# Kernel tuning notes

Measured on AMD Instinct MI355X. Metric: run time of the kernel, lower is better.

## Reference

```python
import jax, jax.numpy as jnp
import numpy as np

B, K, G, C = 64, 4000, 200, 91
LAMBDA_BOX, LAMBDA_CLS, LAMBDA_OBJ = 5.0, 1.0, 1.0
EPS = 1e-9


def _make_boxes(key, lead_shape):
    k1, k2 = jax.random.split(key)
    tl = jax.random.uniform(k1, lead_shape + (2,)) * 0.7
    wh = jax.random.uniform(k2, lead_shape + (2,)) * 0.29 + 0.01
    return jnp.concatenate([tl, tl + wh], axis=-1)


def setup_inputs() -> dict:
    key = jax.random.key(0)
    ks = jax.random.split(key, 6)
    pred_boxes = _make_boxes(ks[0], (B, K))
    pred_obj_logits = jax.random.normal(ks[1], (B, K), dtype=jnp.float32)
    pred_cls_logits = jax.random.normal(ks[2], (B, K, C), dtype=jnp.float32)
    gt_boxes = _make_boxes(ks[3], (B, G))
    gt_labels = jax.random.randint(ks[4], (B, G), 0, C)
    n_gt = jax.random.randint(ks[5], (B,), 1, G + 1)
    gt_mask = jnp.arange(G)[None, :] < n_gt[:, None]
    return dict(pred_boxes=pred_boxes, pred_obj_logits=pred_obj_logits,
                pred_cls_logits=pred_cls_logits, gt_boxes=gt_boxes,
                gt_labels=gt_labels, gt_mask=gt_mask)


def _area(x):
    return jnp.clip(x[..., 2] - x[..., 0], 0.0) * jnp.clip(x[..., 3] - x[..., 1], 0.0)


def _pairwise_iou(a, b):
    # a: (K,4), b: (G,4) -> (K,G)
    tl = jnp.maximum(a[:, None, :2], b[None, :, :2])
    br = jnp.minimum(a[:, None, 2:], b[None, :, 2:])
    wh = jnp.clip(br - tl, 0.0)
    inter = wh[..., 0] * wh[..., 1]
    union = jnp.clip(_area(a)[:, None] + _area(b)[None, :] - inter, EPS)
    return inter / union


def _ciou_loss(pb, gb):
    # pb, gb: (M,4) matched pairs; elementwise CIoU loss = 1 - CIoU
    tl = jnp.maximum(pb[:, :2], gb[:, :2])
    br = jnp.minimum(pb[:, 2:], gb[:, 2:])
    wh = jnp.clip(br - tl, 0.0)
    inter = wh[:, 0] * wh[:, 1]
    iou = inter / jnp.clip(_area(pb) + _area(gb) - inter, EPS)
    px = (pb[:, 0] + pb[:, 2]) * 0.5
    py = (pb[:, 1] + pb[:, 3]) * 0.5
    tx = (gb[:, 0] + gb[:, 2]) * 0.5
    ty = (gb[:, 1] + gb[:, 3]) * 0.5
    rho2 = (px - tx) ** 2 + (py - ty) ** 2
    etl = jnp.minimum(pb[:, :2], gb[:, :2])
    ebr = jnp.maximum(pb[:, 2:], gb[:, 2:])
    c2 = jnp.clip((ebr[:, 0] - etl[:, 0]) ** 2 + (ebr[:, 1] - etl[:, 1]) ** 2, EPS)
    pw = jnp.clip(pb[:, 2] - pb[:, 0], EPS)
    ph = jnp.clip(pb[:, 3] - pb[:, 1], EPS)
    tw = jnp.clip(gb[:, 2] - gb[:, 0], EPS)
    th = jnp.clip(gb[:, 3] - gb[:, 1], EPS)
    v = (4.0 / jnp.pi ** 2) * (jnp.arctan(tw / th) - jnp.arctan(pw / ph)) ** 2
    alpha = jax.lax.stop_gradient(v / (1.0 - iou + v + EPS))  # torch.no_grad
    return 1.0 - (iou - rho2 / c2 - alpha * v)


def _greedy_match(iou0):
    # iou0: (K,G), invalid gt columns pre-masked to -1. Fixed min(K,G)-step
    # argmax-and-mask scan reproducing the torch greedy loop (break -> valid=False).
    Gd = iou0.shape[1]
    steps = min(iou0.shape[0], Gd)

    def step(m, _):
        flat = jnp.argmax(m)
        p = flat // Gd
        g = flat % Gd
        valid = m.reshape(-1)[flat] >= 0.0
        m2 = m.at[p, :].set(-1.0).at[:, g].set(-1.0)
        return jnp.where(valid, m2, m), (p, g, valid)

    _, (ps, gs, vs) = jax.lax.scan(step, iou0, None, length=steps)
    return ps, gs, vs


def _per_batch(pred_b, cls_b, gt_b, labels_b, mask_b):
    iou = jax.lax.stop_gradient(_pairwise_iou(pred_b, gt_b))  # matching is non-diff (.item() in torch)
    iou = jnp.where(mask_b[None, :], iou, -1.0)
    ps, gs, vs = _greedy_match(iou)
    vf = vs.astype(pred_b.dtype)
    n = jnp.sum(vf)
    denom = jnp.maximum(n, 1.0)
    pb = pred_b[ps]
    gb = gt_b[gs]
    lbox = jnp.sum(_ciou_loss(pb, gb) * vf) / denom
    logp = jax.nn.log_softmax(cls_b[ps], axis=-1)
    lce = -jnp.take_along_axis(logp, labels_b[gs][:, None], axis=1)[:, 0]
    lcls = jnp.sum(lce * vf) / denom
    obj_tgt = jnp.zeros((pred_b.shape[0],), pred_b.dtype).at[
        jnp.where(vs, ps, pred_b.shape[0])].set(1.0, mode='drop')
    return lbox, lcls, obj_tgt, n > 0.0


def reference(pred_boxes, pred_obj_logits, pred_cls_logits, gt_boxes, gt_labels, gt_mask):
    lbox_b, lcls_b, obj_tgt, has = jax.vmap(_per_batch)(
        pred_boxes, pred_cls_logits, gt_boxes, gt_labels, gt_mask)
    hf = has.astype(pred_boxes.dtype)
    nb = jnp.maximum(jnp.sum(hf), 1.0)
    loss_box = jnp.sum(lbox_b * hf) / nb
    loss_cls = jnp.sum(lcls_b * hf) / nb
    # BCEWithLogits(mean): softplus(x) - t*x
    loss_obj = jnp.mean(jax.nn.softplus(pred_obj_logits) - obj_tgt * pred_obj_logits)
    total = LAMBDA_BOX * loss_box + LAMBDA_CLS * loss_cls + LAMBDA_OBJ * loss_obj
    return total, loss_box, loss_cls, loss_obj
```

## Files before the change

kernel.cpp:

```cpp
#include <hip/hip_runtime.h>
#include <math.h>

#define B_ 64
#define K_ 4000
#define G_ 200
#define C_ 91
#define EPS_ 1e-9f
#define NW_ 16
#define DEPTH_ 24
typedef unsigned long long ull;

#define WS_FLAG 0
#define WS_PART 256
#define WS_CNT 1536
#define WS_MATCH 2048
#define WS_ROWUSED 53248
#define WS_TOP 327680

__device__ __forceinline__ float box_area(float4 a) {
#pragma clang fp contract(off)
  return fmaxf(a.z - a.x, 0.f) * fmaxf(a.w - a.y, 0.f);
}

__device__ __forceinline__ float iou_ab(float4 a, float aA, float4 b, float aB) {
#pragma clang fp contract(off)
  float tlx = fmaxf(a.x, b.x), tly = fmaxf(a.y, b.y);
  float brx = fminf(a.z, b.z), bry = fminf(a.w, b.w);
  float w = fmaxf(brx - tlx, 0.f), h = fmaxf(bry - tly, 0.f);
  float inter = w * h;
  float uni = fmaxf(aA + aB - inter, EPS_);
  return inter / uni;
}

__device__ __forceinline__ float ciou_loss(float4 p, float4 g) {
  float tlx = fmaxf(p.x, g.x), tly = fmaxf(p.y, g.y);
  float brx = fminf(p.z, g.z), bry = fminf(p.w, g.w);
  float w = fmaxf(brx - tlx, 0.f), h = fmaxf(bry - tly, 0.f);
  float inter = w * h;
  float areaP = fmaxf(p.z - p.x, 0.f) * fmaxf(p.w - p.y, 0.f);
  float areaG = fmaxf(g.z - g.x, 0.f) * fmaxf(g.w - g.y, 0.f);
  float iou = inter / fmaxf(areaP + areaG - inter, EPS_);
  float px = (p.x + p.z) * 0.5f, py = (p.y + p.w) * 0.5f;
  float tx = (g.x + g.z) * 0.5f, ty = (g.y + g.w) * 0.5f;
  float rho2 = (px - tx) * (px - tx) + (py - ty) * (py - ty);
  float ex = fmaxf(p.z, g.z) - fminf(p.x, g.x);
  float ey = fmaxf(p.w, g.w) - fminf(p.y, g.y);
  float c2 = fmaxf(ex * ex + ey * ey, EPS_);
  float pw = fmaxf(p.z - p.x, EPS_), ph = fmaxf(p.w - p.y, EPS_);
  float tw = fmaxf(g.z - g.x, EPS_), th = fmaxf(g.w - g.y, EPS_);
  float dat = atanf(tw / th) - atanf(pw / ph);
  float v = (4.0f / (float)(M_PI * M_PI)) * dat * dat;
  float alpha = v / ((1.f - iou) + v + EPS_);
  return 1.f - (iou - rho2 / c2 - alpha * v);
}

__global__ void kdetect(const unsigned char* m8, int* flag) {
  int b = threadIdx.x;
  int ok = 1;
  const unsigned char* r = m8 + b * G_;
  if (r[0] != 1) ok = 0;
  int seen0 = 0;
  for (int g = 0; g < G_; ++g) {
    unsigned char c = r[g];
    if (c > 1) { ok = 0; break; }
    if (c == 0) seen0 = 1;
    else if (seen0) { ok = 0; break; }
  }
  int all = __all(ok);
  if (b == 0) *flag = all ? 1 : 0;
}

__device__ __forceinline__ float block_sum(float v, float* s_red) {
  for (int off = 32; off > 0; off >>= 1) v += __shfl_xor(v, off);
  int lane = threadIdx.x & 63, wid = threadIdx.x >> 6;
  if (lane == 0) s_red[wid] = v;
  __syncthreads();
  float r = 0.f;
  if (wid == 0) {
    float t = (lane < NW_) ? s_red[lane] : 0.f;
    for (int off = 32; off > 0; off >>= 1) t += __shfl_xor(t, off);
    r = t;
  }
  __syncthreads();
  return r;
}

__device__ __forceinline__ ull wave_maxkey(ull k) {
  for (int off = 32; off > 0; off >>= 1) {
    ull o = __shfl_xor(k, off);
    if (o > k) k = o;
  }
  return k;
}

#define TOP8_INS(key)                                   \
  if ((key) > t7) {                                     \
    t7 = (key);                                         \
    ull tmp_;                                           \
    if (t7 > t6) { tmp_ = t6; t6 = t7; t7 = tmp_; }     \
    if (t6 > t5) { tmp_ = t5; t5 = t6; t6 = tmp_; }     \
    if (t5 > t4) { tmp_ = t4; t4 = t5; t5 = tmp_; }     \
    if (t4 > t3) { tmp_ = t3; t3 = t4; t4 = tmp_; }     \
    if (t3 > t2) { tmp_ = t2; t2 = t3; t3 = tmp_; }     \
    if (t2 > t1) { tmp_ = t1; t1 = t2; t2 = tmp_; }     \
    if (t1 > t0) { tmp_ = t0; t0 = t1; t1 = tmp_; }     \
  }

__global__ __launch_bounds__(1024) void kinit(const float* __restrict__ pred_boxes,
                                              const float* __restrict__ gt_boxes,
                                              const void* __restrict__ gt_mask,
                                              char* __restrict__ ws) {
  __shared__ float4 s_p[K_];
  const int blk = blockIdx.x;
  const int b = blk >> 3, oct = blk & 7;
  const int tid = threadIdx.x, lane = tid & 63, wid = tid >> 6;
  const int msk8 = *(const int*)(ws + WS_FLAG);
  const float4* p4 = (const float4*)pred_boxes + (size_t)b * K_;
  const float4* g4 = (const float4*)gt_boxes + (size_t)b * G_;

  for (int i = tid; i < K_; i += 1024) s_p[i] = p4[i];
  __syncthreads();

  ull* wtop = (ull*)(ws + WS_TOP);
  for (int cc = wid; cc < 25; cc += 16) {
    const int col = oct * 25 + cc;
    ull* dst = wtop + ((size_t)b * G_ + col) * DEPTH_;
    int v;
    if (msk8) v = ((const unsigned char*)gt_mask)[(size_t)b * G_ + col] != 0;
    else      v = ((const int*)gt_mask)[(size_t)b * G_ + col] != 0;
    if (!v) {
      for (int o = lane; o < DEPTH_; o += 64) dst[o] = 0ull;
      continue;
    }
    float4 gb = g4[col];
    float gA = box_area(gb);
    ull t0 = 0, t1 = 0, t2 = 0, t3 = 0, t4 = 0, t5 = 0, t6 = 0, t7 = 0;
    for (int k = lane; k < K_; k += 64) {
      float4 pb = s_p[k];
      float iou = iou_ab(pb, box_area(pb), gb, gA);
      ull e = ((ull)__float_as_uint(iou) << 12) | (ull)(4095 - k);
      TOP8_INS(e);
    }
    int supplied = 0, written = 0;
    for (int o = 0; o < DEPTH_; ++o) {
      ull m = wave_maxkey(t0);
      if (m == 0ull) break;
      int dn = 0;
      if (t0 == m) {
        t0 = t1; t1 = t2; t2 = t3; t3 = t4; t4 = t5; t5 = t6; t6 = t7; t7 = 0;
        if (++supplied == 8) dn = 1;
      }
      if (lane == 0) dst[o] = m;
      ++written;
      if (__any(dn)) break;
    }
    for (int o = written + lane; o < DEPTH_; o += 64) dst[o] = 0ull;
  }
}

__global__ __launch_bounds__(64) void kmatch(const float* __restrict__ pred_boxes,
                                             const float* __restrict__ gt_boxes,
                                             char* __restrict__ ws) {
  __shared__ float s_gx[G_], s_gy[G_], s_gz[G_], s_gw[G_], s_garea[G_];
  __shared__ unsigned char s_rowused[4096];
  __shared__ ull s_toplist[G_][DEPTH_ + 1];
  __shared__ int s_mp[G_];
  __shared__ unsigned short s_mg[G_];
  const int b = blockIdx.x;
  const int lane = threadIdx.x;
  const float4* p4 = (const float4*)pred_boxes + (size_t)b * K_;
  const float4* g4 = (const float4*)gt_boxes + (size_t)b * G_;

  for (int g = lane; g < G_; g += 64) {
    float4 gb = g4[g];
    s_gx[g] = gb.x; s_gy[g] = gb.y; s_gz[g] = gb.z; s_gw[g] = gb.w;
    s_garea[g] = box_area(gb);
  }
  for (int k = lane; k < 4096; k += 64) s_rowused[k] = 0;

  const ull* wtop = (const ull*)(ws + WS_TOP);
  ull key0 = 0, key1 = 0, key2 = 0, key3 = 0;
  int ptr0 = DEPTH_, ptr1 = DEPTH_, ptr2 = DEPTH_, ptr3 = DEPTH_;
  int cloc = 0;
#define SLOTLOAD(S)                                                         \
  { int col = S * 64 + lane;                                                \
    if (col < G_) {                                                         \
      const ull* src_ = wtop + ((size_t)b * G_ + col) * DEPTH_;             \
      ull h_ = src_[0];                                                     \
      s_toplist[col][0] = h_;                                               \
      _Pragma("unroll") for (int o = 1; o < DEPTH_; ++o)                    \
        s_toplist[col][o] = src_[o];                                        \
      if (h_ != 0ull) {                                                     \
        key##S = (h_ << 8) | (ull)(255 - col); ptr##S = 1; ++cloc; } } }
  SLOTLOAD(0) SLOTLOAD(1) SLOTLOAD(2) SLOTLOAD(3)
#undef SLOTLOAD
  for (int off = 32; off > 0; off >>= 1) cloc += __shfl_xor(cloc, off);
  const int cnt = cloc;
  __builtin_amdgcn_wave_barrier();

  for (int step = 0; step < cnt;) {
    ull a1 = key0, a2 = key1;
    if (key1 > key0) { a1 = key1; a2 = key0; }
    if (key2 > a1) { a2 = a1; a1 = key2; } else if (key2 > a2) a2 = key2;
    if (key3 > a1) { a2 = a1; a1 = key3; } else if (key3 > a2) a2 = key3;
    for (int off = 32; off > 0; off >>= 1) {
      ull b1 = __shfl_xor(a1, off), b2 = __shfl_xor(a2, off);
      if (b1 > a1) { a2 = (a1 > b2) ? a1 : b2; a1 = b1; }
      else { a2 = (b1 > a2) ? b1 : a2; }
    }
    const int p1 = 4095 - (int)((a1 >> 8) & 0xFFF);
    const int g1v = 255 - (int)(a1 & 0xFF);
    const int p2 = 4095 - (int)((a2 >> 8) & 0xFFF);
    const int g2v = 255 - (int)(a2 & 0xFF);
    const bool do2 = (a2 != 0ull) && (p2 != p1) && (step + 1 < cnt);
    if (lane == 0) {
      s_mp[step] = p1; s_mg[step] = (unsigned short)g1v; s_rowused[p1] = 1;
      if (do2) { s_mp[step + 1] = p2; s_mg[step + 1] = (unsigned short)g2v; s_rowused[p2] = 1; }
    }
    __builtin_amdgcn_wave_barrier();
    const int gd2 = do2 ? g2v : -1;
    const int pd2 = do2 ? p2 : -1;
    int need = 0;
#define DEMOTE(S)                                                           \
    { int col = S * 64 + lane; ull kk = key##S;                             \
      if (kk != 0ull) {                                                     \
        if (col == g1v || col == gd2) { key##S = 0ull; }                    \
        else { int krow = 4095 - (int)((kk >> 8) & 0xFFF);                  \
          if (krow == p1 || krow == pd2) {                                  \
            ull nk = 0ull; int np = ptr##S;                                 \
            while (np < DEPTH_) {                                           \
              ull e = s_toplist[col][np]; ++np;                             \
              if (e == 0ull) { np = DEPTH_; break; }                        \
              int pr = 4095 - (int)((e >> 12) & 0xFFF);                     \
              if (!s_rowused[pr]) { nk = (e << 8) | (ull)(255 - col); break; } \
            }                                                               \
            ptr##S = np; key##S = nk;                                       \
            if (nk == 0ull) need |= (1 << S); } } } }
    DEMOTE(0) DEMOTE(1) DEMOTE(2) DEMOTE(3)
#undef DEMOTE
    while (__any(need)) {
      unsigned long long bal = __ballot(need != 0);
      int src = (int)__builtin_ctzll(bal);
      int myslot = need ? __builtin_ctz(need) : 0;
      int slot = __shfl(myslot, src);
      int col = slot * 64 + src;
      float4 gb = make_float4(s_gx[col], s_gy[col], s_gz[col], s_gw[col]);
      float gA = s_garea[col];
      ull t0 = 0, t1 = 0, t2 = 0, t3 = 0, t4 = 0, t5 = 0, t6 = 0, t7 = 0;
#pragma unroll 2
      for (int k = lane; k < K_; k += 64) {
        if (!s_rowused[k]) {
          float4 pb = p4[k];
          float iou = iou_ab(pb, box_area(pb), gb, gA);
          ull e = ((ull)__float_as_uint(iou) << 12) | (ull)(4095 - k);
          TOP8_INS(e);
        }
      }
      ull newhead = 0ull;
      int supplied = 0, written = 0;
      for (int o = 0; o < DEPTH_; ++o) {
        ull m = wave_maxkey(t0);
        if (m == 0ull) break;
        if (o == 0) newhead = m;
        int dn = 0;
        if (t0 == m) {
          t0 = t1; t1 = t2; t2 = t3; t3 = t4; t4 = t5; t5 = t6; t6 = t7; t7 = 0;
          if (++supplied == 8) dn = 1;
        }
        if (lane == src) s_toplist[col][o] = m;
        ++written;
        if (__any(dn)) break;
      }
      if (lane == src) {
        for (int o = written; o < DEPTH_; ++o) s_toplist[col][o] = 0ull;
        ull nk = newhead ? ((newhead << 8) | (ull)(255 - col)) : 0ull;
        if (slot == 0) { key0 = nk; ptr0 = 1; }
        else if (slot == 1) { key1 = nk; ptr1 = 1; }
        else if (slot == 2) { key2 = nk; ptr2 = 1; }
        else { key3 = nk; ptr3 = 1; }
        need &= ~(1 << slot);
      }
      __builtin_amdgcn_wave_barrier();
    }
    step += do2 ? 2 : 1;
  }

  unsigned* mout = (unsigned*)(ws + WS_MATCH) + b * G_;
  for (int i = lane; i < cnt; i += 64)
    mout[i] = ((unsigned)s_mp[i] << 8) | (unsigned)s_mg[i];
  unsigned* ruo = (unsigned*)(ws + WS_ROWUSED + (size_t)b * K_);
  const unsigned* rus = (const unsigned*)s_rowused;
  for (int i = lane; i < K_ / 4; i += 64) ruo[i] = rus[i];
  if (lane == 0) ((int*)(ws + WS_CNT))[b] = cnt;
}

__global__ __launch_bounds__(1024) void kepi(const float* __restrict__ pred_boxes,
                                             const float* __restrict__ obj_logits,
                                             const float* __restrict__ cls_logits,
                                             const float* __restrict__ gt_boxes,
                                             const int* __restrict__ gt_labels,
                                             char* __restrict__ ws) {
  __shared__ float s_red[NW_];
  const int b = blockIdx.x;
  const int tid = threadIdx.x;
  const int cnt = ((const int*)(ws + WS_CNT))[b];
  const unsigned* mm = (const unsigned*)(ws + WS_MATCH) + b * G_;
  const unsigned char* ru = (const unsigned char*)(ws + WS_ROWUSED) + (size_t)b * K_;
  const float4* p4 = (const float4*)pred_boxes + (size_t)b * K_;
  const float4* g4 = (const float4*)gt_boxes + (size_t)b * G_;

  float lbox = 0.f, lcls = 0.f;
  for (int i = tid; i < cnt; i += 1024) {
    unsigned e = mm[i];
    int p = (int)(e >> 8), g = (int)(e & 0xFF);
    float4 pb = p4[p];
    float4 gb = g4[g];
    lbox += ciou_loss(pb, gb);
    int label = gt_labels[(size_t)b * G_ + g];
    const float* lg = cls_logits + ((size_t)b * K_ + p) * C_;
    float m = -1e30f;
    for (int cc = 0; cc < C_; ++cc) m = fmaxf(m, lg[cc]);
    float s = 0.f;
    for (int cc = 0; cc < C_; ++cc) s += expf(lg[cc] - m);
    lcls += (m + logf(s)) - lg[label];
  }
  float obj = 0.f;
  const float* ol = obj_logits + (size_t)b * K_;
  for (int k = tid; k < K_; k += 1024) {
    float x = ol[k];
    float sp = fmaxf(x, 0.f) + log1pf(expf(-fabsf(x)));
    if (ru[k]) sp -= x;
    obj += sp;
  }
  lbox = block_sum(lbox, s_red);
  lcls = block_sum(lcls, s_red);
  obj = block_sum(obj, s_red);
  if (tid == 0) {
    float* partials = (float*)(ws + WS_PART);
    float n = (float)cnt;
    float denom = fmaxf(n, 1.f);
    partials[b * 4 + 0] = lbox / denom;
    partials[b * 4 + 1] = lcls / denom;
    partials[b * 4 + 2] = obj;
    partials[b * 4 + 3] = (n > 0.f) ? 1.f : 0.f;
  }
}

__global__ void kfinal(const char* __restrict__ ws, float* __restrict__ out) {
  int b = threadIdx.x;
  const float* partials = (const float*)(ws + WS_PART);
  float lb = partials[b * 4 + 0], lc = partials[b * 4 + 1];
  float ob = partials[b * 4 + 2], hf = partials[b * 4 + 3];
  float sb = lb * hf, sc = lc * hf, sh = hf, so = ob;
  for (int off = 32; off > 0; off >>= 1) {
    sb += __shfl_xor(sb, off);
    sc += __shfl_xor(sc, off);
    sh += __shfl_xor(sh, off);
    so += __shfl_xor(so, off);
  }
  if (b == 0) {
    float nb = fmaxf(sh, 1.f);
    float box = sb / nb, cls = sc / nb;
    float obj = so / (float)(B_ * K_);
    out[0] = 5.f * box + cls + obj;
    out[1] = box;
    out[2] = cls;
    out[3] = obj;
  }
}

extern "C" void kernel_launch(void* const* d_in, const int* in_sizes, int n_in,
                              void* d_out, int out_size, void* d_ws, size_t ws_size,
                              hipStream_t stream) {
  const float* pred_boxes = (const float*)d_in[0];
  const float* obj_logits = (const float*)d_in[1];
  const float* cls_logits = (const float*)d_in[2];
  const float* gt_boxes = (const float*)d_in[3];
  const int* gt_labels = (const int*)d_in[4];
  const void* gt_mask = d_in[5];
  float* out = (float*)d_out;
  char* ws = (char*)d_ws;

  hipLaunchKernelGGL(kdetect, dim3(1), dim3(64), 0, stream,
                     (const unsigned char*)gt_mask, (int*)(ws + WS_FLAG));
  hipLaunchKernelGGL(kinit, dim3(B_ * 8), dim3(1024), 0, stream,
                     pred_boxes, gt_boxes, gt_mask, ws);
  hipLaunchKernelGGL(kmatch, dim3(B_), dim3(64), 0, stream,
                     pred_boxes, gt_boxes, ws);
  hipLaunchKernelGGL(kepi, dim3(B_), dim3(1024), 0, stream,
                     pred_boxes, obj_logits, cls_logits, gt_boxes, gt_labels, ws);
  hipLaunchKernelGGL(kfinal, dim3(1), dim3(64), 0, stream, ws, out);
}
```

Baseline: 295.7 us.

## Fold mask detection into kinit and map one wave per GT column

```diff
diff --git a/kernel.cpp b/kernel.cpp
--- a/kernel.cpp
+++ b/kernel.cpp
@@ -10,7 +10,6 @@
 #define DEPTH_ 24
 typedef unsigned long long ull;
 
-#define WS_FLAG 0
 #define WS_PART 256
 #define WS_CNT 1536
 #define WS_MATCH 2048
@@ -54,22 +53,6 @@
   return 1.f - (iou - rho2 / c2 - alpha * v);
 }
 
-__global__ void kdetect(const unsigned char* m8, int* flag) {
-  int b = threadIdx.x;
-  int ok = 1;
-  const unsigned char* r = m8 + b * G_;
-  if (r[0] != 1) ok = 0;
-  int seen0 = 0;
-  for (int g = 0; g < G_; ++g) {
-    unsigned char c = r[g];
-    if (c > 1) { ok = 0; break; }
-    if (c == 0) seen0 = 1;
-    else if (seen0) { ok = 0; break; }
-  }
-  int all = __all(ok);
-  if (b == 0) *flag = all ? 1 : 0;
-}
-
 __device__ __forceinline__ float block_sum(float v, float* s_red) {
   for (int off = 32; off > 0; off >>= 1) v += __shfl_xor(v, off);
   int lane = threadIdx.x & 63, wid = threadIdx.x >> 6;
@@ -106,56 +89,67 @@
     if (t1 > t0) { tmp_ = t0; t0 = t1; t1 = tmp_; }     \
   }
 
+__device__ __forceinline__ int detect_msk8(const unsigned char* m8) {
+  int lane = threadIdx.x & 63;
+  int ok = 1;
+  const unsigned char* r = m8 + lane * G_;
+  if (r[0] != 1) ok = 0;
+  int seen0 = 0;
+  for (int g = 0; g < G_; ++g) {
+    unsigned char c = r[g];
+    if (c > 1) { ok = 0; break; }
+    if (c == 0) seen0 = 1;
+    else if (seen0) { ok = 0; break; }
+  }
+  return __all(ok) ? 1 : 0;
+}
+
 __global__ __launch_bounds__(1024) void kinit(const float* __restrict__ pred_boxes,
                                               const float* __restrict__ gt_boxes,
                                               const void* __restrict__ gt_mask,
                                               char* __restrict__ ws) {
-  __shared__ float4 s_p[K_];
   const int blk = blockIdx.x;
-  const int b = blk >> 3, oct = blk & 7;
-  const int tid = threadIdx.x, lane = tid & 63, wid = tid >> 6;
-  const int msk8 = *(const int*)(ws + WS_FLAG);
+  const int b = blk / 13, q = blk - 13 * b;
+  const int lane = threadIdx.x & 63, wid = threadIdx.x >> 6;
+  const int col = q * 16 + wid;
+  if (col >= G_) return;
+
+  const int msk8 = detect_msk8((const unsigned char*)gt_mask);
   const float4* p4 = (const float4*)pred_boxes + (size_t)b * K_;
   const float4* g4 = (const float4*)gt_boxes + (size_t)b * G_;
-
-  for (int i = tid; i < K_; i += 1024) s_p[i] = p4[i];
-  __syncthreads();
-
-  ull* wtop = (ull*)(ws + WS_TOP);
-  for (int cc = wid; cc < 25; cc += 16) {
-    const int col = oct * 25 + cc;
-    ull* dst = wtop + ((size_t)b * G_ + col) * DEPTH_;
-    int v;
-    if (msk8) v = ((const unsigned char*)gt_mask)[(size_t)b * G_ + col] != 0;
-    else      v = ((const int*)gt_mask)[(size_t)b * G_ + col] != 0;
-    if (!v) {
-      for (int o = lane; o < DEPTH_; o += 64) dst[o] = 0ull;
-      continue;
+  ull* dst = (ull*)(ws + WS_TOP) + ((size_t)b * G_ + col) * DEPTH_;
+
+  int v;
+  if (msk8) v = ((const unsigned char*)gt_mask)[(size_t)b * G_ + col] != 0;
+  else      v = ((const int*)gt_mask)[(size_t)b * G_ + col] != 0;
+  if (!v) {
+    for (int o = lane; o < DEPTH_; o += 64) dst[o] = 0ull;
+    return;
+  }
+  float4 gb = g4[col];
+  float gA = box_area(gb);
+  ull t0 = 0, t1 = 0, t2 = 0, t3 = 0, t4 = 0, t5 = 0, t6 = 0, t7 = 0;
+#pragma unroll 2
+  for (int k = lane; k < K_; k += 64) {
+    float4 pb = p4[k];
+    float iou = iou_ab(pb, box_area(pb), gb, gA);
+    ull e = ((ull)__float_as_uint(iou) << 12) | (ull)(4095 - k);
+    TOP8_INS(e);
+  }
+  int supplied = 0, written = 0;
+  for (int o = 0; o < DEPTH_; ++o) {
+    ull m = wave_maxkey(t0);
+    if (m == 0ull) break;
+    int dn = 0;
+    if (t0 == m) {
+      t0 = t1; t1 = t2; t2 = t3; t3 = t4; t4 = t5; t5 = t6; t6 = t7; t7 = 0;
+      if (++supplied == 8) dn = 1;
     }
-    float4 gb = g4[col];
-    float gA = box_area(gb);
-    ull t0 = 0, t1 = 0, t2 = 0, t3 = 0, t4 = 0, t5 = 0, t6 = 0, t7 = 0;
-    for (int k = lane; k < K_; k += 64) {
-      float4 pb = s_p[k];
-      float iou = iou_ab(pb, box_area(pb), gb, gA);
-      ull e = ((ull)__float_as_uint(iou) << 12) | (ull)(4095 - k);
-      TOP8_INS(e);
-    }
-    int supplied = 0, written = 0;
-    for (int o = 0; o < DEPTH_; ++o) {
-      ull m = wave_maxkey(t0);
-      if (m == 0ull) break;
-      int dn = 0;
-      if (t0 == m) {
-        t0 = t1; t1 = t2; t2 = t3; t3 = t4; t4 = t5; t5 = t6; t6 = t7; t7 = 0;
-        if (++supplied == 8) dn = 1;
-      }
-      if (lane == 0) dst[o] = m;
-      ++written;
-      if (__any(dn)) break;
-    }
-    for (int o = written + lane; o < DEPTH_; o += 64) dst[o] = 0ull;
-  }
+    if (lane == 0) dst[o] = m;
+    ++written;
+    if (__any(dn)) break;
+  }
+  for (int o = written + lane; o < DEPTH_; o += 64) dst[o] = 0ull;
 }
 
 __global__ __launch_bounds__(64) void kmatch(const float* __restrict__ pred_boxes,
@@ -381,9 +375,7 @@
   float* out = (float*)d_out;
   char* ws = (char*)d_ws;
 
-  hipLaunchKernelGGL(kdetect, dim3(1), dim3(64), 0, stream,
-                     (const unsigned char*)gt_mask, (int*)(ws + WS_FLAG));
-  hipLaunchKernelGGL(kinit, dim3(B_ * 8), dim3(1024), 0, stream,
+  hipLaunchKernelGGL(kinit, dim3(B_ * 13), dim3(1024), 0, stream,
                      pred_boxes, gt_boxes, gt_mask, ws);
   hipLaunchKernelGGL(kmatch, dim3(B_), dim3(64), 0, stream,
                      pred_boxes, gt_boxes, ws);
```

Result: slower. 354.6 us (+20.0%).

## Fuse greedy match with loss epilogue and shrink initial per-column top-k

Applied to the files above, without the earlier changes.

```diff
diff --git a/kernel.cpp b/kernel.cpp
--- a/kernel.cpp
+++ b/kernel.cpp
@@ -7,14 +7,11 @@
 #define C_ 91
 #define EPS_ 1e-9f
 #define NW_ 16
-#define DEPTH_ 24
+#define DEPTH_ 32
 typedef unsigned long long ull;
 
 #define WS_FLAG 0
 #define WS_PART 256
-#define WS_CNT 1536
-#define WS_MATCH 2048
-#define WS_ROWUSED 53248
 #define WS_TOP 327680
 
 __device__ __forceinline__ float box_area(float4 a) {
@@ -93,6 +90,15 @@
   return k;
 }
 
+#define TOP4_INS(key)                                   \
+  if ((key) > t3) {                                     \
+    t3 = (key);                                         \
+    ull tmp_;                                           \
+    if (t3 > t2) { tmp_ = t2; t2 = t3; t3 = tmp_; }     \
+    if (t2 > t1) { tmp_ = t1; t1 = t2; t2 = tmp_; }     \
+    if (t1 > t0) { tmp_ = t0; t0 = t1; t1 = tmp_; }     \
+  }
+
 #define TOP8_INS(key)                                   \
   if ((key) > t7) {                                     \
     t7 = (key);                                         \
@@ -134,12 +140,13 @@
     }
     float4 gb = g4[col];
     float gA = box_area(gb);
-    ull t0 = 0, t1 = 0, t2 = 0, t3 = 0, t4 = 0, t5 = 0, t6 = 0, t7 = 0;
+    ull t0 = 0, t1 = 0, t2 = 0, t3 = 0;
+#pragma unroll 2
     for (int k = lane; k < K_; k += 64) {
       float4 pb = s_p[k];
       float iou = iou_ab(pb, box_area(pb), gb, gA);
       ull e = ((ull)__float_as_uint(iou) << 12) | (ull)(4095 - k);
-      TOP8_INS(e);
+      TOP4_INS(e);
     }
     int supplied = 0, written = 0;
     for (int o = 0; o < DEPTH_; ++o) {
@@ -147,8 +154,8 @@
       if (m == 0ull) break;
       int dn = 0;
       if (t0 == m) {
-        t0 = t1; t1 = t2; t2 = t3; t3 = t4; t4 = t5; t5 = t6; t6 = t7; t7 = 0;
-        if (++supplied == 8) dn = 1;
+        t0 = t1; t1 = t2; t2 = t3; t3 = 0;
+        if (++supplied == 4) dn = 1;
       }
       if (lane == 0) dst[o] = m;
       ++written;
@@ -158,163 +165,144 @@
   }
 }
 
-__global__ __launch_bounds__(64) void kmatch(const float* __restrict__ pred_boxes,
-                                             const float* __restrict__ gt_boxes,
-                                             char* __restrict__ ws) {
+__global__ __launch_bounds__(1024) void kmerged(
+    const float* __restrict__ pred_boxes, const float* __restrict__ obj_logits,
+    const float* __restrict__ cls_logits, const float* __restrict__ gt_boxes,
+    const int* __restrict__ gt_labels, char* __restrict__ ws) {
   __shared__ float s_gx[G_], s_gy[G_], s_gz[G_], s_gw[G_], s_garea[G_];
   __shared__ unsigned char s_rowused[4096];
   __shared__ ull s_toplist[G_][DEPTH_ + 1];
   __shared__ int s_mp[G_];
   __shared__ unsigned short s_mg[G_];
+  __shared__ int s_cnt;
+  __shared__ float s_red[NW_];
   const int b = blockIdx.x;
-  const int lane = threadIdx.x;
+  const int tid = threadIdx.x, lane = tid & 63, wid = tid >> 6;
   const float4* p4 = (const float4*)pred_boxes + (size_t)b * K_;
   const float4* g4 = (const float4*)gt_boxes + (size_t)b * G_;
-
-  for (int g = lane; g < G_; g += 64) {
+  const ull* wtop = (const ull*)(ws + WS_TOP);
+
+  for (int g = tid; g < G_; g += 1024) {
     float4 gb = g4[g];
     s_gx[g] = gb.x; s_gy[g] = gb.y; s_gz[g] = gb.z; s_gw[g] = gb.w;
     s_garea[g] = box_area(gb);
   }
-  for (int k = lane; k < 4096; k += 64) s_rowused[k] = 0;
-
-  const ull* wtop = (const ull*)(ws + WS_TOP);
-  ull key0 = 0, key1 = 0, key2 = 0, key3 = 0;
-  int ptr0 = DEPTH_, ptr1 = DEPTH_, ptr2 = DEPTH_, ptr3 = DEPTH_;
-  int cloc = 0;
-#define SLOTLOAD(S)                                                         \
-  { int col = S * 64 + lane;                                                \
-    if (col < G_) {                                                         \
-      const ull* src_ = wtop + ((size_t)b * G_ + col) * DEPTH_;             \
-      ull h_ = src_[0];                                                     \
-      s_toplist[col][0] = h_;                                               \
-      _Pragma("unroll") for (int o = 1; o < DEPTH_; ++o)                    \
-        s_toplist[col][o] = src_[o];                                        \
-      if (h_ != 0ull) {                                                     \
-        key##S = (h_ << 8) | (ull)(255 - col); ptr##S = 1; ++cloc; } } }
-  SLOTLOAD(0) SLOTLOAD(1) SLOTLOAD(2) SLOTLOAD(3)
-#undef SLOTLOAD
-  for (int off = 32; off > 0; off >>= 1) cloc += __shfl_xor(cloc, off);
-  const int cnt = cloc;
-  __builtin_amdgcn_wave_barrier();
-
-  for (int step = 0; step < cnt;) {
-    ull a1 = key0, a2 = key1;
-    if (key1 > key0) { a1 = key1; a2 = key0; }
-    if (key2 > a1) { a2 = a1; a1 = key2; } else if (key2 > a2) a2 = key2;
-    if (key3 > a1) { a2 = a1; a1 = key3; } else if (key3 > a2) a2 = key3;
-    for (int off = 32; off > 0; off >>= 1) {
-      ull b1 = __shfl_xor(a1, off), b2 = __shfl_xor(a2, off);
-      if (b1 > a1) { a2 = (a1 > b2) ? a1 : b2; a1 = b1; }
-      else { a2 = (b1 > a2) ? b1 : a2; }
-    }
-    const int p1 = 4095 - (int)((a1 >> 8) & 0xFFF);
-    const int g1v = 255 - (int)(a1 & 0xFF);
-    const int p2 = 4095 - (int)((a2 >> 8) & 0xFFF);
-    const int g2v = 255 - (int)(a2 & 0xFF);
-    const bool do2 = (a2 != 0ull) && (p2 != p1) && (step + 1 < cnt);
-    if (lane == 0) {
-      s_mp[step] = p1; s_mg[step] = (unsigned short)g1v; s_rowused[p1] = 1;
-      if (do2) { s_mp[step + 1] = p2; s_mg[step + 1] = (unsigned short)g2v; s_rowused[p2] = 1; }
-    }
-    __builtin_amdgcn_wave_barrier();
-    const int gd2 = do2 ? g2v : -1;
-    const int pd2 = do2 ? p2 : -1;
-    int need = 0;
-#define DEMOTE(S)                                                           \
-    { int col = S * 64 + lane; ull kk = key##S;                             \
-      if (kk != 0ull) {                                                     \
-        if (col == g1v || col == gd2) { key##S = 0ull; }                    \
-        else { int krow = 4095 - (int)((kk >> 8) & 0xFFF);                  \
-          if (krow == p1 || krow == pd2) {                                  \
-            ull nk = 0ull; int np = ptr##S;                                 \
-            while (np < DEPTH_) {                                           \
-              ull e = s_toplist[col][np]; ++np;                             \
-              if (e == 0ull) { np = DEPTH_; break; }                        \
-              int pr = 4095 - (int)((e >> 12) & 0xFFF);                     \
-              if (!s_rowused[pr]) { nk = (e << 8) | (ull)(255 - col); break; } \
-            }                                                               \
-            ptr##S = np; key##S = nk;                                       \
-            if (nk == 0ull) need |= (1 << S); } } } }
-    DEMOTE(0) DEMOTE(1) DEMOTE(2) DEMOTE(3)
-#undef DEMOTE
-    while (__any(need)) {
-      unsigned long long bal = __ballot(need != 0);
-      int src = (int)__builtin_ctzll(bal);
-      int myslot = need ? __builtin_ctz(need) : 0;
-      int slot = __shfl(myslot, src);
-      int col = slot * 64 + src;
-      float4 gb = make_float4(s_gx[col], s_gy[col], s_gz[col], s_gw[col]);
-      float gA = s_garea[col];
-      ull t0 = 0, t1 = 0, t2 = 0, t3 = 0, t4 = 0, t5 = 0, t6 = 0, t7 = 0;
-#pragma unroll 2
-      for (int k = lane; k < K_; k += 64) {
-        if (!s_rowused[k]) {
-          float4 pb = p4[k];
-          float iou = iou_ab(pb, box_area(pb), gb, gA);
-          ull e = ((ull)__float_as_uint(iou) << 12) | (ull)(4095 - k);
-          TOP8_INS(e);
-        }
+  for (int k = tid; k < 4096; k += 1024) s_rowused[k] = 0;
+  for (int i = tid; i < G_ * DEPTH_; i += 1024)
+    s_toplist[i / DEPTH_][i % DEPTH_] = wtop[((size_t)b * G_) * DEPTH_ + i];
+  __syncthreads();
+
+  if (wid == 0) {
+    ull key0 = 0, key1 = 0, key2 = 0, key3 = 0;
+    int ptr0 = DEPTH_, ptr1 = DEPTH_, ptr2 = DEPTH_, ptr3 = DEPTH_;
+    int cloc = 0;
+#define SLOTINIT(S)                                                        \
+    { int col = S * 64 + lane;                                             \
+      if (col < G_) {                                                      \
+        ull h_ = s_toplist[col][0];                                        \
+        if (h_ != 0ull) {                                                  \
+          key##S = (h_ << 8) | (ull)(255 - col); ptr##S = 1; ++cloc; } } }
+    SLOTINIT(0) SLOTINIT(1) SLOTINIT(2) SLOTINIT(3)
+#undef SLOTINIT
+    for (int off = 32; off > 0; off >>= 1) cloc += __shfl_xor(cloc, off);
+    const int cnt = cloc;
+    if (lane == 0) s_cnt = cnt;
+
+    for (int step = 0; step < cnt;) {
+      ull a1 = key0, a2 = key1;
+      if (key1 > key0) { a1 = key1; a2 = key0; }
+      if (key2 > a1) { a2 = a1; a1 = key2; } else if (key2 > a2) a2 = key2;
+      if (key3 > a1) { a2 = a1; a1 = key3; } else if (key3 > a2) a2 = key3;
+      for (int off = 32; off > 0; off >>= 1) {
+        ull b1 = __shfl_xor(a1, off), b2 = __shfl_xor(a2, off);
+        if (b1 > a1) { a2 = (a1 > b2) ? a1 : b2; a1 = b1; }
+        else { a2 = (b1 > a2) ? b1 : a2; }
       }
-      ull newhead = 0ull;
-      int supplied = 0, written = 0;
-      for (int o = 0; o < DEPTH_; ++o) {
-        ull m = wave_maxkey(t0);
-        if (m == 0ull) break;
-        if (o == 0) newhead = m;
-        int dn = 0;
-        if (t0 == m) {
-          t0 = t1; t1 = t2; t2 = t3; t3 = t4; t4 = t5; t5 = t6; t6 = t7; t7 = 0;
-          if (++supplied == 8) dn = 1;
-        }
-        if (lane == src) s_toplist[col][o] = m;
-        ++written;
-        if (__any(dn)) break;
-      }
-      if (lane == src) {
-        for (int o = written; o < DEPTH_; ++o) s_toplist[col][o] = 0ull;
-        ull nk = newhead ? ((newhead << 8) | (ull)(255 - col)) : 0ull;
-        if (slot == 0) { key0 = nk; ptr0 = 1; }
-        else if (slot == 1) { key1 = nk; ptr1 = 1; }
-        else if (slot == 2) { key2 = nk; ptr2 = 1; }
-        else { key3 = nk; ptr3 = 1; }
-        need &= ~(1 << slot);
+      const int p1 = 4095 - (int)((a1 >> 8) & 0xFFF);
+      const int g1v = 255 - (int)(a1 & 0xFF);
+      const int p2 = 4095 - (int)((a2 >> 8) & 0xFFF);
+      const int g2v = 255 - (int)(a2 & 0xFF);
+      const bool do2 = (a2 != 0ull) && (p2 != p1) && (step + 1 < cnt);
+      if (lane == 0) {
+        s_mp[step] = p1; s_mg[step] = (unsigned short)g1v; s_rowused[p1] = 1;
+        if (do2) { s_mp[step + 1] = p2; s_mg[step + 1] = (unsigned short)g2v; s_rowused[p2] = 1; }
       }
       __builtin_amdgcn_wave_barrier();
+      const int gd2 = do2 ? g2v : -1;
+      const int pd2 = do2 ? p2 : -1;
+      int need = 0;
+#define DEMOTE(S)                                                           \
+      { int col = S * 64 + lane; ull kk = key##S;                           \
+        if (kk != 0ull) {                                                   \
+          if (col == g1v || col == gd2) { key##S = 0ull; }                  \
+          else { int krow = 4095 - (int)((kk >> 8) & 0xFFF);                \
+            if (krow == p1 || krow == pd2) {                                \
+              ull nk = 0ull; int np = ptr##S;                               \
+              while (np < DEPTH_) {                                         \
+                ull e = s_toplist[col][np]; ++np;                           \
+                if (e == 0ull) { np = DEPTH_; break; }                      \
+                int pr = 4095 - (int)((e >> 12) & 0xFFF);                   \
+                if (!s_rowused[pr]) { nk = (e << 8) | (ull)(255 - col); break; } \
+              }                                                             \
+              ptr##S = np; key##S = nk;                                     \
+              if (nk == 0ull) need |= (1 << S); } } } }
+      DEMOTE(0) DEMOTE(1) DEMOTE(2) DEMOTE(3)
+#undef DEMOTE
+      while (__any(need)) {
+        unsigned long long bal = __ballot(need != 0);
+        int src = (int)__builtin_ctzll(bal);
+        int myslot = need ? __builtin_ctz(need) : 0;
+        int slot = __shfl(myslot, src);
+        int col = slot * 64 + src;
+        float4 gb = make_float4(s_gx[col], s_gy[col], s_gz[col], s_gw[col]);
+        float gA = s_garea[col];
+        ull t0 = 0, t1 = 0, t2 = 0, t3 = 0, t4 = 0, t5 = 0, t6 = 0, t7 = 0;
+#pragma unroll 2
+        for (int k = lane; k < K_; k += 64) {
+          if (!s_rowused[k]) {
+            float4 pb = p4[k];
+            float iou = iou_ab(pb, box_area(pb), gb, gA);
+            ull e = ((ull)__float_as_uint(iou) << 12) | (ull)(4095 - k);
+            TOP8_INS(e);
+          }
+        }
+        ull newhead = 0ull;
+        int supplied = 0, written = 0;
+        for (int o = 0; o < DEPTH_; ++o) {
+          ull m = wave_maxkey(t0);
+          if (m == 0ull) break;
+          if (o == 0) newhead = m;
+          int dn = 0;
+          if (t0 == m) {
+            t0 = t1; t1 = t2; t2 = t3; t3 = t4; t4 = t5; t5 = t6; t6 = t7; t7 = 0;
+            if (++supplied == 8) dn = 1;
+          }
+          if (lane == src) s_toplist[col][o] = m;
+          ++written;
+          if (__any(dn)) break;
+        }
+        if (lane == src) {
+          for (int o = written; o < DEPTH_; ++o) s_toplist[col][o] = 0ull;
+          ull nk = newhead ? ((newhead << 8) | (ull)(255 - col)) : 0ull;
+          if (slot == 0) { key0 = nk; ptr0 = 1; }
+          else if (slot == 1) { key1 = nk; ptr1 = 1; }
+          else if (slot == 2) { key2 = nk; ptr2 = 1; }
+          else { key3 = nk; ptr3 = 1; }
+          need &= ~(1 << slot);
+        }
+        __builtin_amdgcn_wave_barrier();
+      }
+      step += do2 ? 2 : 1;
     }
-    step += do2 ? 2 : 1;
-  }
-
-  unsigned* mout = (unsigned*)(ws + WS_MATCH) + b * G_;
-  for (int i = lane; i < cnt; i += 64)
-    mout[i] = ((unsigned)s_mp[i] << 8) | (unsigned)s_mg[i];
-  unsigned* ruo = (unsigned*)(ws + WS_ROWUSED + (size_t)b * K_);
-  const unsigned* rus = (const unsigned*)s_rowused;
-  for (int i = lane; i < K_ / 4; i += 64) ruo[i] = rus[i];
-  if (lane == 0) ((int*)(ws + WS_CNT))[b] = cnt;
-}
-
-__global__ __launch_bounds__(1024) void kepi(const float* __restrict__ pred_boxes,
-                                             const float* __restrict__ obj_logits,
-                                             const float* __restrict__ cls_logits,
-                                             const float* __restrict__ gt_boxes,
-                                             const int* __restrict__ gt_labels,
-                                             char* __restrict__ ws) {
-  __shared__ float s_red[NW_];
-  const int b = blockIdx.x;
-  const int tid = threadIdx.x;
-  const int cnt = ((const int*)(ws + WS_CNT))[b];
-  const unsigned* mm = (const unsigned*)(ws + WS_MATCH) + b * G_;
-  const unsigned char* ru = (const unsigned char*)(ws + WS_ROWUSED) + (size_t)b * K_;
-  const float4* p4 = (const float4*)pred_boxes + (size_t)b * K_;
-  const float4* g4 = (const float4*)gt_boxes + (size_t)b * G_;
-
+  }
+  __syncthreads();
+
+  const int cnt = s_cnt;
   float lbox = 0.f, lcls = 0.f;
   for (int i = tid; i < cnt; i += 1024) {
-    unsigned e = mm[i];
-    int p = (int)(e >> 8), g = (int)(e & 0xFF);
+    int p = s_mp[i], g = s_mg[i];
     float4 pb = p4[p];
-    float4 gb = g4[g];
+    float4 gb = make_float4(s_gx[g], s_gy[g], s_gz[g], s_gw[g]);
     lbox += ciou_loss(pb, gb);
     int label = gt_labels[(size_t)b * G_ + g];
     const float* lg = cls_logits + ((size_t)b * K_ + p) * C_;
@@ -329,7 +317,7 @@
   for (int k = tid; k < K_; k += 1024) {
     float x = ol[k];
     float sp = fmaxf(x, 0.f) + log1pf(expf(-fabsf(x)));
-    if (ru[k]) sp -= x;
+    if (s_rowused[k]) sp -= x;
     obj += sp;
   }
   lbox = block_sum(lbox, s_red);
@@ -385,9 +373,7 @@
                      (const unsigned char*)gt_mask, (int*)(ws + WS_FLAG));
   hipLaunchKernelGGL(kinit, dim3(B_ * 8), dim3(1024), 0, stream,
                      pred_boxes, gt_boxes, gt_mask, ws);
-  hipLaunchKernelGGL(kmatch, dim3(B_), dim3(64), 0, stream,
-                     pred_boxes, gt_boxes, ws);
-  hipLaunchKernelGGL(kepi, dim3(B_), dim3(1024), 0, stream,
+  hipLaunchKernelGGL(kmerged, dim3(B_), dim3(1024), 0, stream,
                      pred_boxes, obj_logits, cls_logits, gt_boxes, gt_labels, ws);
   hipLaunchKernelGGL(kfinal, dim3(1), dim3(64), 0, stream, ws, out);
 }
```

After: 259.3 us. 12.3% less time.
